# Kernel tuning notes

Hardware: AMD Instinct MI355X
Metric: run time of the kernel (lower is better)

The kernel has to match this reference:

```python
import jax, jax.numpy as jnp
import numpy as np

NEG_INF = -1.0e9  # masked_fill value used by the torch module
LN_EPS = 1e-6


def setup_inputs() -> dict:
    key = jax.random.key(0)
    ks = jax.random.split(key, 10)
    B, S, D = 4, 1024, 1024
    H, DK, DV = 16, 64, 64
    q = jax.random.normal(ks[0], (B, S, D), dtype=jnp.float32)
    k = jax.random.normal(ks[1], (B, S, D), dtype=jnp.float32)
    v = jax.random.normal(ks[2], (B, S, D), dtype=jnp.float32)
    mask = jax.random.randint(ks[3], (B, S, S), 0, 2, dtype=jnp.int32)
    sc = 1.0 / np.sqrt(D)
    wq = jax.random.normal(ks[4], (H, D, DK), dtype=jnp.float32) * sc  # per-head W_qs stacked
    wk = jax.random.normal(ks[5], (H, D, DK), dtype=jnp.float32) * sc
    wv = jax.random.normal(ks[6], (H, D, DV), dtype=jnp.float32) * sc
    fc_w = jax.random.normal(ks[7], (D, H * DV), dtype=jnp.float32) * (1.0 / np.sqrt(H * DV))  # torch Linear weight [out,in]
    ln_g = jnp.ones((D,), dtype=jnp.float32)
    ln_b = jnp.zeros((D,), dtype=jnp.float32)
    return {"q": q, "k": k, "v": v, "mask": mask, "wq": wq, "wk": wk,
            "wv": wv, "fc_w": fc_w, "ln_g": ln_g, "ln_b": ln_b}


def reference(q, k, v, mask, wq, wk, wv, fc_w, ln_g, ln_b):
    # Batched equivalent of the per-head Python loop (dropout in eval mode = identity).
    B, S, D = q.shape
    H, _, DK = wq.shape
    DV = wv.shape[-1]
    temperature = jnp.asarray(DK, q.dtype) ** 0.5
    residual = q
    qh = jnp.einsum('bqd,hdk->bhqk', q, wq)   # [B,H,Q,DK]
    kh = jnp.einsum('bsd,hdk->bhsk', k, wk)   # [B,H,K,DK]
    vh = jnp.einsum('bsd,hdv->bhsv', v, wv)   # [B,H,K,DV]
    attn = jnp.einsum('bhqe,bhke->bhqk', qh / temperature, kh)  # [B,H,Q,K]
    attn = jnp.where(mask[:, None, :, :] == 0, jnp.asarray(NEG_INF, attn.dtype), attn)
    attn = jax.nn.softmax(attn, axis=-1)
    heads = jnp.einsum('bhqk,bhkv->bhqv', attn, vh)             # [B,H,Q,DV]
    # concat heads along feature dim in head order (matches torch.cat of the loop outputs)
    concat = jnp.transpose(heads, (0, 2, 1, 3)).reshape(B, S, H * DV)
    out = concat @ fc_w.T                                        # fc, no bias
    out = out + residual
    mu = jnp.mean(out, axis=-1, keepdims=True)
    var = jnp.mean(jnp.square(out - mu), axis=-1, keepdims=True)
    out = (out - mu) / jnp.sqrt(var + LN_EPS) * ln_g + ln_b
    return out
```

## Files before the change

### kernel.cpp

```cpp
#include <hip/hip_runtime.h>
#include <hip/hip_bf16.h>

typedef __bf16 bf16x8 __attribute__((ext_vector_type(8)));
typedef __bf16 bf16x4 __attribute__((ext_vector_type(4)));
typedef __bf16 bf16x2 __attribute__((ext_vector_type(2)));
typedef float f32x4 __attribute__((ext_vector_type(4)));
typedef unsigned int u32x2 __attribute__((ext_vector_type(2)));

#define MFMA16(a, b, c) __builtin_amdgcn_mfma_f32_16x16x32_bf16(a, b, c, 0, 0, 0)

static constexpr int M_ = 4096;

__device__ __forceinline__ void gload_lds16(const void* g, void* l) {
  __builtin_amdgcn_global_load_lds((const __attribute__((address_space(1))) void*)g,
                                   (__attribute__((address_space(3))) void*)l, 16, 0, 0);
}

__device__ __forceinline__ float exp2_hw(float x) {
  float r;
  asm("v_exp_f32 %0, %1" : "=v"(r) : "v"(x));
  return r;
}

__device__ __forceinline__ bf16x8 cvt8(float4 x, float4 y) {
  bf16x8 o;
  o[0] = (__bf16)x.x; o[1] = (__bf16)x.y; o[2] = (__bf16)x.z; o[3] = (__bf16)x.w;
  o[4] = (__bf16)y.x; o[5] = (__bf16)y.y; o[6] = (__bf16)y.z; o[7] = (__bf16)y.w;
  return o;
}

#define SWZ(rowv, c16) (((rowv) * 64) + (((c16) ^ ((rowv) & 7)) * 8))

__global__ __launch_bounds__(256) void prep(const float* __restrict__ fc_w,
                                            const float* __restrict__ wq,
                                            const float* __restrict__ wk,
                                            const float* __restrict__ wv,
                                            const int* __restrict__ mask,
                                            __bf16* __restrict__ WFC,
                                            __bf16* __restrict__ W3T,
                                            unsigned long long* __restrict__ bits) {
  __shared__ float tile[64][65];
  int bx = blockIdx.x;
  const int t = threadIdx.x;

  if (bx < 512) {
    int i = bx * 256 + t;
    const float4* p = (const float4*)fc_w + (size_t)i * 2;
    float4 a = p[0], b = p[1];
    *((bf16x8*)WFC + i) = cvt8(a, b);
    return;
  }
  bx -= 512;
  if (bx < 768) {
    const int z = bx >> 8, rem = bx & 255;
    const float* w = z == 0 ? wq : (z == 1 ? wk : wv);
    const float scale = z == 0 ? 0.125f * 1.4426950408889634f : 1.0f;
    __bf16* o = W3T + (size_t)z * 1048576;
    const int h = rem & 15, d0 = (rem >> 4) * 64;
    const int r = t >> 2, c0 = (t & 3) * 16;
    const float4* s4 = (const float4*)(w + ((size_t)h * 1024 + d0 + r) * 64 + c0);
#pragma unroll
    for (int j = 0; j < 4; ++j) {
      float4 vv = s4[j];
      tile[r][c0 + 4 * j + 0] = vv.x; tile[r][c0 + 4 * j + 1] = vv.y;
      tile[r][c0 + 4 * j + 2] = vv.z; tile[r][c0 + 4 * j + 3] = vv.w;
    }
    __syncthreads();
    __bf16* dst = o + ((size_t)(h * 64 + r)) * 1024 + d0 + c0;
    bf16x8 o0, o1;
#pragma unroll
    for (int j = 0; j < 8; ++j) o0[j] = (__bf16)(tile[c0 + j][r] * scale);
#pragma unroll
    for (int j = 0; j < 8; ++j) o1[j] = (__bf16)(tile[c0 + 8 + j][r] * scale);
    *(bf16x8*)dst = o0;
    *(bf16x8*)(dst + 8) = o1;
    return;
  }
  bx -= 768;
  {
    const int wid = bx * 4 + (t >> 6);
    const int lane = t & 63;
#pragma unroll
    for (int i = 0; i < 16; ++i) {
      int widx = wid * 16 + i;
      int qrow = widx & 1023;
      int bkt = widx >> 10;
      int b = bkt >> 4, kt = bkt & 15;
      int mval = mask[((size_t)b * 1024 + qrow) * 1024 + kt * 64 + lane];
      unsigned long long bal = __ballot(mval != 0);
      if (lane == 0) bits[widx] = bal;
    }
  }
}

__global__ __launch_bounds__(256) void gemm_qkv(const float* __restrict__ q,
                                                const float* __restrict__ k,
                                                const float* __restrict__ v,
                                                const __bf16* __restrict__ Btbase,
                                                __bf16* __restrict__ HEADS) {
  __shared__ __bf16 SMEM[16384];
  const int L = blockIdx.x;
  const int wl = (L & 7) * 96 + (L >> 3);
  const int bn = wl & 7;
  const int bmz = wl >> 3;
  const int bm = bmz & 31, z = bmz >> 5;
  const float* Af = z == 0 ? q : (z == 1 ? k : v);
  const __bf16* Bt = Btbase + (size_t)z * 1048576;
  const int tid = threadIdx.x, lane = tid & 63;
  const int w = tid >> 6;
  const int wr = (w >> 1) * 64, wc = (w & 1) * 64;
  const int lr = lane & 15, lh = lane >> 4;

  const int rowA = tid >> 2, colf = (tid & 3) * 8;
  const float* gA0 = Af + (size_t)(bm * 128 + rowA) * 1024 + colf;
  const float* gA1 = gA0 + 64 * 1024;
  const int o0 = tid * 16;
  const int row0 = o0 >> 6, cb = o0 & 63;
  const char* apB0 = (const char*)Bt + ((size_t)(bn * 128 + row0) * 1024) * 2 + cb;
  const char* apB1 = apB0 + 64 * 2048;
  char* smemB = (char*)SMEM + 16384;

#define BSTAGE(buf)                                         \
  do {                                                      \
    char* dd = smemB + (buf) * 8192;                        \
    gload_lds16(apB0, dd + o0);                             \
    gload_lds16(apB1, dd + 4096 + o0);                      \
    apB0 += 64; apB1 += 64;                                 \
  } while (0)

  f32x4 acc[4][4];
#pragma unroll
  for (int m = 0; m < 4; ++m)
#pragma unroll
    for (int n = 0; n < 4; ++n) {
      f32x4 zz = {0.f, 0.f, 0.f, 0.f};
      acc[m][n] = zz;
    }

  {
    float4 a0 = *(const float4*)gA0, a1 = *(const float4*)(gA0 + 4);
    float4 b0 = *(const float4*)gA1, b1 = *(const float4*)(gA1 + 4);
    gA0 += 32; gA1 += 32;
    *(bf16x8*)((char*)SMEM + o0) = cvt8(a0, a1);
    *(bf16x8*)((char*)SMEM + 4096 + o0) = cvt8(b0, b1);
  }
  BSTAGE(0);
  __syncthreads();

  for (int kt = 0; kt < 32; ++kt) {
    const int cur = kt & 1;
    float4 a0, a1, b0, b1;
    if (kt < 31) {
      a0 = *(const float4*)gA0; a1 = *(const float4*)(gA0 + 4);
      b0 = *(const float4*)gA1; b1 = *(const float4*)(gA1 + 4);
      gA0 += 32; gA1 += 32;
      BSTAGE(cur ^ 1);
    }
    __builtin_amdgcn_sched_barrier(0);
    const int ab = cur * 4096;
    const int bb = 8192 + cur * 4096;
    bf16x8 af[4], bfr[4];
#pragma unroll
    for (int m = 0; m < 4; ++m)
      af[m] = *(const bf16x8*)&SMEM[ab + (wr + m * 16 + lr) * 32 + lh * 8];
#pragma unroll
    for (int n = 0; n < 4; ++n)
      bfr[n] = *(const bf16x8*)&SMEM[bb + (wc + n * 16 + lr) * 32 + lh * 8];
    __builtin_amdgcn_s_setprio(1);
#pragma unroll
    for (int m = 0; m < 4; ++m)
#pragma unroll
      for (int n = 0; n < 4; ++n) acc[m][n] = MFMA16(af[m], bfr[n], acc[m][n]);
    __builtin_amdgcn_s_setprio(0);
    __builtin_amdgcn_sched_barrier(0);
    if (kt < 31) {
      char* dA = (char*)SMEM + (cur ^ 1) * 8192;
      *(bf16x8*)(dA + o0) = cvt8(a0, a1);
      *(bf16x8*)(dA + 4096 + o0) = cvt8(b0, b1);
    }
    __syncthreads();
  }
#undef BSTAGE

  if (z == 2) {
    const int hl = w & 1;
    const size_t vtbase = 2ull * 4194304;
    const size_t bb2 = (size_t)(bm >> 3) * 16 + bn * 2;
    const int kkbase = (bm & 7) * 128;
#pragma unroll
    for (int p = 0; p < 2; ++p) {
      if (hl == p) {
#pragma unroll
        for (int m = 0; m < 4; ++m)
#pragma unroll
          for (int n = 0; n < 4; ++n) {
            const int dk = n * 16 + lr;
            const int s = wr + m * 16 + lh * 4;
            bf16x4 pv;
#pragma unroll
            for (int j = 0; j < 4; ++j) pv[j] = (__bf16)acc[m][n][j];
            *(bf16x4*)&SMEM[dk * 132 + s] = pv;
          }
      }
      __syncthreads();
      {
        const int dk = tid >> 2, sc = tid & 3;
        const __bf16* srcp = &SMEM[dk * 132 + sc * 32];
        __bf16* dstp = HEADS + vtbase + ((bb2 + p) * 64 + dk) * 1024 + kkbase + sc * 32;
#pragma unroll
        for (int u = 0; u < 8; ++u) *(bf16x4*)(dstp + u * 4) = *(const bf16x4*)(srcp + u * 4);
      }
      __syncthreads();
    }
    return;
  }

#pragma unroll
  for (int p = 0; p < 2; ++p) {
    if ((w >> 1) == p) {
#pragma unroll
      for (int m = 0; m < 4; ++m)
#pragma unroll
        for (int n = 0; n < 4; ++n)
#pragma unroll
          for (int reg = 0; reg < 4; ++reg)
            SMEM[(m * 16 + lh * 4 + reg) * 132 + wc + n * 16 + lr] = (__bf16)acc[m][n][reg];
    }
    __syncthreads();
    {
      const int rowl = tid >> 2, c0 = (tid & 3) * 32;
      const int row = bm * 128 + p * 64 + rowl;
      const int b = row >> 10, s = row & 1023;
      const int h = bn * 2 + (c0 >> 6), dk0 = c0 & 63;
      __bf16* dst = HEADS + (size_t)z * 4194304 + (((size_t)b * 16 + h) * 1024 + s) * 64 + dk0;
      const __bf16* srcp = &SMEM[rowl * 132 + c0];
#pragma unroll
      for (int u = 0; u < 8; ++u) *(bf16x4*)(dst + u * 4) = *(const bf16x4*)(srcp + u * 4);
    }
    __syncthreads();
  }
}

__global__ __launch_bounds__(256) void gemm_fc64(const __bf16* __restrict__ A,
                                                 const __bf16* __restrict__ Bt,
                                                 __bf16* __restrict__ O,
                                                 const float* __restrict__ resid) {
  __shared__ __bf16 SMEM[12288];
  const int L = blockIdx.x;
  const int wl = (L & 7) * 64 + (L >> 3);
  const int bn = wl & 7, bm = wl >> 3;
  const int tid = threadIdx.x, lane = tid & 63;
  const int w = tid >> 6;
  const int wc = w * 32;
  const int lr = lane & 15, lh = lane >> 4;

  const int o0 = tid * 16;
  const int row0 = o0 >> 6, cb = o0 & 63;
  const char* apA = (const char*)A + ((size_t)(bm * 64 + row0) * 1024) * 2 + cb;
  const char* apB0 = (const char*)Bt + ((size_t)(bn * 128 + row0) * 1024) * 2 + cb;
  const char* apB1 = apB0 + 64 * 2048;
  char* smem = (char*)SMEM;

#define FSTAGE(buf)                                         \
  do {                                                      \
    gload_lds16(apA, smem + (buf) * 4096 + o0);             \
    char* dd = smem + 8192 + (buf) * 8192;                  \
    gload_lds16(apB0, dd + o0);                             \
    gload_lds16(apB1, dd + 4096 + o0);                      \
    apA += 64; apB0 += 64; apB1 += 64;                      \
  } while (0)

  f32x4 acc[4][2];
#pragma unroll
  for (int m = 0; m < 4; ++m)
#pragma unroll
    for (int n = 0; n < 2; ++n) {
      f32x4 z = {0.f, 0.f, 0.f, 0.f};
      acc[m][n] = z;
    }

  FSTAGE(0);
  __syncthreads();

  for (int kt = 0; kt < 32; ++kt) {
    const int cur = kt & 1;
    if (kt < 31) FSTAGE(cur ^ 1);
    const int ab = cur * 2048;
    const int bb = 4096 + cur * 4096;
    bf16x8 af[4], bfr[2];
#pragma unroll
    for (int m = 0; m < 4; ++m) af[m] = *(const bf16x8*)&SMEM[ab + (m * 16 + lr) * 32 + lh * 8];
#pragma unroll
    for (int n = 0; n < 2; ++n)
      bfr[n] = *(const bf16x8*)&SMEM[bb + (wc + n * 16 + lr) * 32 + lh * 8];
    __builtin_amdgcn_s_setprio(1);
#pragma unroll
    for (int m = 0; m < 4; ++m)
#pragma unroll
      for (int n = 0; n < 2; ++n) acc[m][n] = MFMA16(af[m], bfr[n], acc[m][n]);
    __builtin_amdgcn_s_setprio(0);
    __syncthreads();
  }
#undef FSTAGE

#pragma unroll
  for (int m = 0; m < 4; ++m)
#pragma unroll
    for (int n = 0; n < 2; ++n)
#pragma unroll
      for (int reg = 0; reg < 4; ++reg) {
        int row = bm * 64 + m * 16 + lh * 4 + reg;
        int col = bn * 128 + wc + n * 16 + lr;
        size_t idx = (size_t)row * 1024 + col;
        O[idx] = (__bf16)(acc[m][n][reg] + resid[idx]);
      }
}

__global__ __launch_bounds__(256, 4) void attn_kernel(const __bf16* __restrict__ HEADS,
                                                      const unsigned long long* __restrict__ m64,
                                                      __bf16* __restrict__ concat) {
  const __bf16* QH = HEADS;
  const __bf16* KH = HEADS + (size_t)M_ * 1024;
  const __bf16* VT = HEADS + (size_t)2 * M_ * 1024;
  __shared__ __bf16 Ks[2][2][32 * 64];
  __shared__ __bf16 Vs[2][2][64 * 32];
  __shared__ unsigned Psw[2][4][256];

  const int d = blockIdx.x;
  const int xcd = d & 7, j = d >> 3;
  const int grp = xcd * 8 + (j >> 4);
  const int qt = j & 15;
  const int h = grp & 15, b = grp >> 4;

  const int tid = threadIdx.x, lane = tid & 63, w = tid >> 6;
  const int lr = lane & 15, lh = lane >> 4;
  const size_t headoff = ((size_t)b * 16 + h) * 65536;
  const char* Kbase = (const char*)(KH + headoff);
  const char* Vbase = (const char*)(VT + headoff);

  const int krow = tid >> 3, kg = tid & 7;
  const int kgo = krow * 128 + ((kg ^ (krow & 7)) * 16);
  const int vrow = tid >> 2, vg = tid & 3;
  const int vgo = vrow * 2048 + ((vg ^ ((vrow >> 1) & 3)) * 16);
  const int ldsb = tid * 16;

  const char* kpA = Kbase + kgo;
  const char* kpB = Kbase + 65536 + kgo;
  const char* vpA = Vbase + vgo;
  const char* vpB = Vbase + 1024 + vgo;

#define STAGE(buf)                                          \
  do {                                                      \
    gload_lds16(kpA, (char*)Ks[buf][0] + ldsb);             \
    gload_lds16(kpB, (char*)Ks[buf][1] + ldsb);             \
    gload_lds16(vpA, (char*)Vs[buf][0] + ldsb);             \
    gload_lds16(vpB, (char*)Vs[buf][1] + ldsb);             \
    kpA += 4096; kpB += 4096; vpA += 64; vpB += 64;         \
  } while (0)

  const int qrow = qt * 64 + w * 16 + lr;
  bf16x8 qa[2];
  {
    const __bf16* qptr = QH + headoff + (size_t)qrow * 64 + lh * 8;
    qa[0] = *(const bf16x8*)qptr;
    qa[1] = *(const bf16x8*)(qptr + 32);
  }
  f32x4 oacc[4];
#pragma unroll
  for (int g = 0; g < 4; ++g) {
    f32x4 z = {0.f, 0.f, 0.f, 0.f};
    oacc[g] = z;
  }
  float lrun = 0.f;

  const unsigned long long* m64A = m64 + (size_t)b * 16384 + qrow;
  const unsigned long long* m64B = m64A + 8192;
  unsigned long long pairA = m64A[0], pairB = m64B[0];
  unsigned long long pairAn = 0, pairBn = 0;

  const int vcol = (lh ^ ((lr >> 1) & 3)) * 8;
  const int pread = lr * 32 + vcol;
  const int pG = (lr >> 1) & 3;
  int kread[2][2], vread[4];
#pragma unroll
  for (int n = 0; n < 2; ++n)
#pragma unroll
    for (int h2 = 0; h2 < 2; ++h2) kread[n][h2] = SWZ(n * 16 + lr, h2 * 4 + lh);
#pragma unroll
  for (int g = 0; g < 4; ++g) vread[g] = (g * 16 + lr) * 32 + vcol;

  STAGE(0);
  __syncthreads();

#pragma unroll 2
  for (int t = 0; t < 16; ++t) {
    const int cur = t & 1;
    if ((t & 1) == 0 && t < 14) {
      pairAn = m64A[((t >> 1) + 1) * 1024];
      pairBn = m64B[((t >> 1) + 1) * 1024];
    }
    const unsigned mwA = (t & 1) ? (unsigned)(pairA >> 32) : (unsigned)pairA;
    const unsigned mwB = (t & 1) ? (unsigned)(pairB >> 32) : (unsigned)pairB;
    if (t < 15) STAGE(cur ^ 1);

    f32x4 sA[2], sB[2];
#pragma unroll
    for (int n = 0; n < 2; ++n) {
      f32x4 z = {0.f, 0.f, 0.f, 0.f};
      sA[n] = z; sB[n] = z;
    }
    __builtin_amdgcn_s_setprio(1);
#pragma unroll
    for (int n = 0; n < 2; ++n)
#pragma unroll
      for (int h2 = 0; h2 < 2; ++h2) {
        bf16x8 kbA = *(const bf16x8*)&Ks[cur][0][kread[n][h2]];
        bf16x8 kbB = *(const bf16x8*)&Ks[cur][1][kread[n][h2]];
        sA[n] = MFMA16(kbA, qa[h2], sA[n]);
        sB[n] = MFMA16(kbB, qa[h2], sB[n]);
      }
    __builtin_amdgcn_s_setprio(0);

#pragma unroll
    for (int n = 0; n < 2; ++n)
#pragma unroll
      for (int r = 0; r < 4; ++r) {
        unsigned bit = (mwA >> (n * 16 + lh * 4 + r)) & 1u;
        float p = bit ? exp2_hw(sA[n][r]) : 0.0f;
        sA[n][r] = p;
        lrun += p;
      }
#pragma unroll
    for (int n = 0; n < 2; ++n)
#pragma unroll
      for (int r = 0; r < 4; ++r) {
        unsigned bit = (mwB >> (n * 16 + lh * 4 + r)) & 1u;
        float p = bit ? exp2_hw(sB[n][r]) : 0.0f;
        sB[n][r] = p;
        lrun += p;
      }

#pragma unroll
    for (int n = 0; n < 2; ++n) {
      bf16x2 p0, p1;
      p0[0] = (__bf16)sA[n][0]; p0[1] = (__bf16)sA[n][1];
      p1[0] = (__bf16)sA[n][2]; p1[1] = (__bf16)sA[n][3];
      int G = n * 2 + (lh >> 1);
      int addr = lr * 16 + ((G ^ pG) * 4) + (lh & 1) * 2;
      u32x2 wv;
      wv[0] = __builtin_bit_cast(unsigned, p0);
      wv[1] = __builtin_bit_cast(unsigned, p1);
      *(u32x2*)&Psw[0][w][addr] = wv;
    }
#pragma unroll
    for (int n = 0; n < 2; ++n) {
      bf16x2 p0, p1;
      p0[0] = (__bf16)sB[n][0]; p0[1] = (__bf16)sB[n][1];
      p1[0] = (__bf16)sB[n][2]; p1[1] = (__bf16)sB[n][3];
      int G = n * 2 + (lh >> 1);
      int addr = lr * 16 + ((G ^ pG) * 4) + (lh & 1) * 2;
      u32x2 wv;
      wv[0] = __builtin_bit_cast(unsigned, p0);
      wv[1] = __builtin_bit_cast(unsigned, p1);
      *(u32x2*)&Psw[1][w][addr] = wv;
    }
    bf16x8 paA = *(const bf16x8*)&((const __bf16*)Psw[0][w])[pread];
    bf16x8 paB = *(const bf16x8*)&((const __bf16*)Psw[1][w])[pread];

    __builtin_amdgcn_s_setprio(1);
#pragma unroll
    for (int g = 0; g < 4; ++g) {
      bf16x8 vbA = *(const bf16x8*)&Vs[cur][0][vread[g]];
      bf16x8 vbB = *(const bf16x8*)&Vs[cur][1][vread[g]];
      oacc[g] = MFMA16(paA, vbA, oacc[g]);
      oacc[g] = MFMA16(paB, vbB, oacc[g]);
    }
    __builtin_amdgcn_s_setprio(0);
    if (t & 1) { pairA = pairAn; pairB = pairBn; }
    __syncthreads();
  }
#undef STAGE

  lrun += __shfl_xor(lrun, 16, 64);
  lrun += __shfl_xor(lrun, 32, 64);
  const float linv = 1.0f / (lrun + 1e-30f);
  const int qg0 = qt * 64 + w * 16 + lh * 4;
#pragma unroll
  for (int r = 0; r < 4; ++r) {
    const float ir = __shfl(linv, (lane & 48) | (lh * 4 + r), 64);
#pragma unroll
    for (int g = 0; g < 4; ++g)
      concat[((size_t)b * 1024 + qg0 + r) * 1024 + h * 64 + g * 16 + lr] =
          (__bf16)(oacc[g][r] * ir);
  }
}

__global__ __launch_bounds__(256) void ln_kernel(const __bf16* __restrict__ in,
                                                 const float* __restrict__ gam,
                                                 const float* __restrict__ bet,
                                                 float* __restrict__ out) {
  const int row = blockIdx.x, t = threadIdx.x;
  bf16x4 xv = *((const bf16x4*)(in + (size_t)row * 1024) + t);
  float x0 = (float)xv[0], x1 = (float)xv[1], x2 = (float)xv[2], x3 = (float)xv[3];
  float s = x0 + x1 + x2 + x3;
  float sq = x0 * x0 + x1 * x1 + x2 * x2 + x3 * x3;
#pragma unroll
  for (int off = 1; off < 64; off <<= 1) {
    s += __shfl_xor(s, off, 64);
    sq += __shfl_xor(sq, off, 64);
  }
  __shared__ float red[8];
  const int w = t >> 6, lane = t & 63;
  if (lane == 0) { red[w] = s; red[4 + w] = sq; }
  __syncthreads();
  s = red[0] + red[1] + red[2] + red[3];
  sq = red[4] + red[5] + red[6] + red[7];
  const float mu = s * (1.0f / 1024.0f);
  const float var = sq * (1.0f / 1024.0f) - mu * mu;
  const float rstd = rsqrtf(var + 1e-6f);
  float4 g4 = ((const float4*)gam)[t];
  float4 b4 = ((const float4*)bet)[t];
  float4 o;
  o.x = (x0 - mu) * rstd * g4.x + b4.x;
  o.y = (x1 - mu) * rstd * g4.y + b4.y;
  o.z = (x2 - mu) * rstd * g4.z + b4.z;
  o.w = (x3 - mu) * rstd * g4.w + b4.w;
  ((float4*)(out + (size_t)row * 1024))[t] = o;
}

extern "C" void kernel_launch(void* const* d_in, const int* in_sizes, int n_in,
                              void* d_out, int out_size, void* d_ws, size_t ws_size,
                              hipStream_t stream) {
  (void)in_sizes; (void)n_in; (void)out_size; (void)ws_size;
  const float* q = (const float*)d_in[0];
  const float* k = (const float*)d_in[1];
  const float* v = (const float*)d_in[2];
  const int* mask = (const int*)d_in[3];
  const float* wq = (const float*)d_in[4];
  const float* wk = (const float*)d_in[5];
  const float* wv = (const float*)d_in[6];
  const float* fc_w = (const float*)d_in[7];
  const float* ln_g = (const float*)d_in[8];
  const float* ln_b = (const float*)d_in[9];
  float* out = (float*)d_out;

  __bf16* QKVBF = (__bf16*)d_ws;
  __bf16* W3T   = QKVBF + 3ull * 4194304;
  __bf16* WFC   = W3T + 3ull * 1048576;
  __bf16* HEADS = WFC + 1048576;
  __bf16* CONCAT = HEADS + 3ull * 4194304;
  __bf16* OUT1B = CONCAT + 4194304;
  unsigned long long* MASKB = (unsigned long long*)(OUT1B + 4194304);

  prep<<<2304, 256, 0, stream>>>(fc_w, wq, wk, wv, mask, WFC, W3T, MASKB);
  gemm_qkv<<<768, 256, 0, stream>>>(q, k, v, W3T, HEADS);
  attn_kernel<<<1024, 256, 0, stream>>>(HEADS, MASKB, CONCAT);
  gemm_fc64<<<512, 256, 0, stream>>>(CONCAT, WFC, OUT1B, q);
  ln_kernel<<<4096, 256, 0, stream>>>(OUT1B, ln_g, ln_b, out);
}
```

Baseline: 111.3 us.

## Widen QKV GEMM tile to 128x256 with 512-thread blocks

The QKV projection GEMM moves from 128x128 tiles with 256 threads to 128x256 tiles with 512 threads (8 waves), halving the grid to 384 blocks. Each fp32 A tile is now loaded and converted to bf16 once per 256 output columns, which halves the redundant A reads and conversions. B fragments are loaded per n-iteration inside the MFMA loop, and the epilogues are restructured to write four-head chunks. In exchange, LDS use per block is larger and there are fewer blocks to fill the GPU's compute units.

Result: faster. 107.3 us (median of 2 runs) (-3.5%).

```diff
diff --git a/kernel.cpp b/kernel.cpp
--- a/kernel.cpp
+++ b/kernel.cpp
@@ -93,39 +93,37 @@
   }
 }
 
-__global__ __launch_bounds__(256) void gemm_qkv(const float* __restrict__ q,
+__global__ __launch_bounds__(512) void gemm_qkv(const float* __restrict__ q,
                                                 const float* __restrict__ k,
                                                 const float* __restrict__ v,
                                                 const __bf16* __restrict__ Btbase,
                                                 __bf16* __restrict__ HEADS) {
-  __shared__ __bf16 SMEM[16384];
+  __shared__ __bf16 SMEM[24576];
   const int L = blockIdx.x;
-  const int wl = (L & 7) * 96 + (L >> 3);
-  const int bn = wl & 7;
-  const int bmz = wl >> 3;
-  const int bm = bmz & 31, z = bmz >> 5;
+  const int wl = (L & 7) * 48 + (L >> 3);
+  const int bnp = wl & 3;
+  const int rem = wl >> 2;
+  const int bm = rem & 31, z = rem >> 5;
   const float* Af = z == 0 ? q : (z == 1 ? k : v);
   const __bf16* Bt = Btbase + (size_t)z * 1048576;
   const int tid = threadIdx.x, lane = tid & 63;
   const int w = tid >> 6;
-  const int wr = (w >> 1) * 64, wc = (w & 1) * 64;
+  const int wr = (w >> 2) * 64;
+  const int wcl = (w & 3) * 64;
   const int lr = lane & 15, lh = lane >> 4;
-
-  const int rowA = tid >> 2, colf = (tid & 3) * 8;
-  const float* gA0 = Af + (size_t)(bm * 128 + rowA) * 1024 + colf;
-  const float* gA1 = gA0 + 64 * 1024;
+  char* smem = (char*)SMEM;
   const int o0 = tid * 16;
-  const int row0 = o0 >> 6, cb = o0 & 63;
-  const char* apB0 = (const char*)Bt + ((size_t)(bn * 128 + row0) * 1024) * 2 + cb;
-  const char* apB1 = apB0 + 64 * 2048;
-  char* smemB = (char*)SMEM + 16384;
-
-#define BSTAGE(buf)                                         \
-  do {                                                      \
-    char* dd = smemB + (buf) * 8192;                        \
-    gload_lds16(apB0, dd + o0);                             \
-    gload_lds16(apB1, dd + 4096 + o0);                      \
-    apB0 += 64; apB1 += 64;                                 \
+
+  const float* gA = Af + (size_t)(bm * 128 + (tid >> 2)) * 1024 + (tid & 3) * 8;
+  const char* apB = (const char*)Bt + ((size_t)(bnp * 256 + (tid >> 2)) * 1024) * 2 +
+                    (tid & 3) * 16;
+
+#define BSTAGE(buf)                                           \
+  do {                                                        \
+    char* db = smem + 16384 + (buf) * 16384;                  \
+    gload_lds16(apB, db + o0);                                \
+    gload_lds16(apB + 262144, db + 8192 + o0);                \
+    apB += 64;                                                \
   } while (0)
 
   f32x4 acc[4][4];
@@ -138,58 +136,52 @@
     }
 
   {
-    float4 a0 = *(const float4*)gA0, a1 = *(const float4*)(gA0 + 4);
-    float4 b0 = *(const float4*)gA1, b1 = *(const float4*)(gA1 + 4);
-    gA0 += 32; gA1 += 32;
-    *(bf16x8*)((char*)SMEM + o0) = cvt8(a0, a1);
-    *(bf16x8*)((char*)SMEM + 4096 + o0) = cvt8(b0, b1);
+    float4 a0 = *(const float4*)gA, a1 = *(const float4*)(gA + 4);
+    gA += 32;
+    *(bf16x8*)(smem + o0) = cvt8(a0, a1);
   }
   BSTAGE(0);
   __syncthreads();
 
   for (int kt = 0; kt < 32; ++kt) {
     const int cur = kt & 1;
-    float4 a0, a1, b0, b1;
+    float4 a0, a1;
     if (kt < 31) {
-      a0 = *(const float4*)gA0; a1 = *(const float4*)(gA0 + 4);
-      b0 = *(const float4*)gA1; b1 = *(const float4*)(gA1 + 4);
-      gA0 += 32; gA1 += 32;
+      a0 = *(const float4*)gA; a1 = *(const float4*)(gA + 4);
+      gA += 32;
       BSTAGE(cur ^ 1);
     }
     __builtin_amdgcn_sched_barrier(0);
     const int ab = cur * 4096;
-    const int bb = 8192 + cur * 4096;
-    bf16x8 af[4], bfr[4];
+    const int bb = 8192 + cur * 8192;
+    bf16x8 af[4];
 #pragma unroll
     for (int m = 0; m < 4; ++m)
       af[m] = *(const bf16x8*)&SMEM[ab + (wr + m * 16 + lr) * 32 + lh * 8];
-#pragma unroll
-    for (int n = 0; n < 4; ++n)
-      bfr[n] = *(const bf16x8*)&SMEM[bb + (wc + n * 16 + lr) * 32 + lh * 8];
     __builtin_amdgcn_s_setprio(1);
 #pragma unroll
-    for (int m = 0; m < 4; ++m)
-#pragma unroll
-      for (int n = 0; n < 4; ++n) acc[m][n] = MFMA16(af[m], bfr[n], acc[m][n]);
+    for (int n = 0; n < 4; ++n) {
+      bf16x8 bfr = *(const bf16x8*)&SMEM[bb + (wcl + n * 16 + lr) * 32 + lh * 8];
+#pragma unroll
+      for (int m = 0; m < 4; ++m) acc[m][n] = MFMA16(af[m], bfr, acc[m][n]);
+    }
     __builtin_amdgcn_s_setprio(0);
     __builtin_amdgcn_sched_barrier(0);
     if (kt < 31) {
-      char* dA = (char*)SMEM + (cur ^ 1) * 8192;
+      char* dA = smem + (cur ^ 1) * 8192;
       *(bf16x8*)(dA + o0) = cvt8(a0, a1);
-      *(bf16x8*)(dA + 4096 + o0) = cvt8(b0, b1);
     }
     __syncthreads();
   }
 #undef BSTAGE
 
   if (z == 2) {
-    const int hl = w & 1;
     const size_t vtbase = 2ull * 4194304;
-    const size_t bb2 = (size_t)(bm >> 3) * 16 + bn * 2;
+    const size_t bbh = (size_t)(bm >> 3) * 16 + bnp * 4;
     const int kkbase = (bm & 7) * 128;
 #pragma unroll
-    for (int p = 0; p < 2; ++p) {
-      if (hl == p) {
+    for (int p = 0; p < 4; ++p) {
+      if ((w & 3) == p) {
 #pragma unroll
         for (int m = 0; m < 4; ++m)
 #pragma unroll
@@ -204,11 +196,11 @@
       }
       __syncthreads();
       {
-        const int dk = tid >> 2, sc = tid & 3;
-        const __bf16* srcp = &SMEM[dk * 132 + sc * 32];
-        __bf16* dstp = HEADS + vtbase + ((bb2 + p) * 64 + dk) * 1024 + kkbase + sc * 32;
-#pragma unroll
-        for (int u = 0; u < 8; ++u) *(bf16x4*)(dstp + u * 4) = *(const bf16x4*)(srcp + u * 4);
+        const int dk = tid >> 3, sc = tid & 7;
+        const __bf16* srcp = &SMEM[dk * 132 + sc * 16];
+        __bf16* dstp = HEADS + vtbase + ((bbh + p) * 64 + dk) * 1024 + kkbase + sc * 16;
+#pragma unroll
+        for (int u = 0; u < 4; ++u) *(bf16x4*)(dstp + u * 4) = *(const bf16x4*)(srcp + u * 4);
       }
       __syncthreads();
     }
@@ -216,29 +208,34 @@
   }
 
 #pragma unroll
-  for (int p = 0; p < 2; ++p) {
-    if ((w >> 1) == p) {
-#pragma unroll
-      for (int m = 0; m < 4; ++m)
-#pragma unroll
-        for (int n = 0; n < 4; ++n)
-#pragma unroll
-          for (int reg = 0; reg < 4; ++reg)
-            SMEM[(m * 16 + lh * 4 + reg) * 132 + wc + n * 16 + lr] = (__bf16)acc[m][n][reg];
-    }
-    __syncthreads();
-    {
-      const int rowl = tid >> 2, c0 = (tid & 3) * 32;
-      const int row = bm * 128 + p * 64 + rowl;
-      const int b = row >> 10, s = row & 1023;
-      const int h = bn * 2 + (c0 >> 6), dk0 = c0 & 63;
-      __bf16* dst = HEADS + (size_t)z * 4194304 + (((size_t)b * 16 + h) * 1024 + s) * 64 + dk0;
-      const __bf16* srcp = &SMEM[rowl * 132 + c0];
-#pragma unroll
-      for (int u = 0; u < 8; ++u) *(bf16x4*)(dst + u * 4) = *(const bf16x4*)(srcp + u * 4);
-    }
-    __syncthreads();
-  }
+  for (int p = 0; p < 2; ++p)
+#pragma unroll
+    for (int ph = 0; ph < 2; ++ph) {
+      if ((w >> 2) == p && ((w >> 1) & 1) == ph) {
+        const int colbase = (w & 1) * 64;
+#pragma unroll
+        for (int m = 0; m < 4; ++m)
+#pragma unroll
+          for (int n = 0; n < 4; ++n)
+#pragma unroll
+            for (int reg = 0; reg < 4; ++reg)
+              SMEM[(m * 16 + lh * 4 + reg) * 132 + colbase + n * 16 + lr] =
+                  (__bf16)acc[m][n][reg];
+      }
+      __syncthreads();
+      {
+        const int rowl = tid >> 3, c0 = (tid & 7) * 16;
+        const int row = bm * 128 + p * 64 + rowl;
+        const int b_ = row >> 10, s = row & 1023;
+        const int col = bnp * 256 + ph * 128 + c0;
+        const int h = col >> 6, dk0 = col & 63;
+        __bf16* dst = HEADS + (size_t)z * 4194304 + (((size_t)b_ * 16 + h) * 1024 + s) * 64 + dk0;
+        const __bf16* srcp = &SMEM[rowl * 132 + c0];
+#pragma unroll
+        for (int u = 0; u < 4; ++u) *(bf16x4*)(dst + u * 4) = *(const bf16x4*)(srcp + u * 4);
+      }
+      __syncthreads();
+    }
 }
 
 __global__ __launch_bounds__(256) void gemm_fc64(const __bf16* __restrict__ A,
@@ -553,7 +550,7 @@
   unsigned long long* MASKB = (unsigned long long*)(OUT1B + 4194304);
 
   prep<<<2304, 256, 0, stream>>>(fc_w, wq, wk, wv, mask, WFC, W3T, MASKB);
-  gemm_qkv<<<768, 256, 0, stream>>>(q, k, v, W3T, HEADS);
+  gemm_qkv<<<384, 512, 0, stream>>>(q, k, v, W3T, HEADS);
   attn_kernel<<<1024, 256, 0, stream>>>(HEADS, MASKB, CONCAT);
   gemm_fc64<<<512, 256, 0, stream>>>(CONCAT, WFC, OUT1B, q);
   ln_kernel<<<4096, 256, 0, stream>>>(OUT1B, ln_g, ln_b, out);
```
